# Optimization experiments

Hardware: AMD Instinct MI355X
Metric: run time of the kernel (lower is better)

## Reference

```python
import jax, jax.numpy as jnp
import numpy as np
from jax import lax

TAU = 2.0
VTH = 1.0
T = 4

def heaviside(x):
    return (x >= 0.0).astype(x.dtype)

def lif_step(v, x):
    # decay_input=False, v_reset=0: v <- v*(1-1/tau) + x ; hard reset to 0
    v = v * (1.0 - 1.0 / TAU) + x
    s = heaviside(v - VTH)
    v = v * (1.0 - s)
    return v, s

def setup_inputs() -> dict:
    key = jax.random.key(0)
    k = jax.random.split(key, 5)
    B, H, W3, W4 = 128, 64, 8, 32
    cc, N, O = 8, 512, 16
    flat = cc * H * W3 * W4  # 131072
    x = jax.random.normal(k[0], (B, 2, H, W3, W4), dtype=jnp.float32)
    w_conv = jax.random.normal(k[1], (cc, 2, 3, 3), dtype=jnp.float32) / np.sqrt(2 * 9)
    w1 = jax.random.normal(k[2], (N, flat), dtype=jnp.float32) / np.sqrt(flat)
    w2 = jax.random.normal(k[3], (N, N), dtype=jnp.float32) / np.sqrt(N)
    w_out = jax.random.normal(k[4], (O, N), dtype=jnp.float32) / np.sqrt(N)
    return {"x": x, "w_conv": w_conv, "w1": w1, "w2": w2, "w_out": w_out}

def reference(x, w_conv, w1, w2, w_out):
    B = x.shape[0]
    # input.reshape(B, C, -1, W4)
    xr = x.reshape(B, x.shape[1], -1, x.shape[4])  # (B, 2, 512, 32)
    conv_input = lax.conv_general_dilated(
        xr, w_conv, window_strides=(1, 1), padding="SAME",
        dimension_numbers=("NCHW", "OIHW", "NCHW"))  # (B, cc, 512, 32)

    # lifconv applied T times to the same conv_input with persistent state
    def conv_step(v, _):
        return lif_step(v, conv_input)
    _, conv_spikes = lax.scan(conv_step, jnp.zeros_like(conv_input), None, length=T)  # (T,B,cc,H',W')

    N = w1.shape[0]
    def fc_step(carry, s_conv):
        v1, v2 = carry
        z1 = s_conv.reshape(B, -1) @ w1.T
        v1, s1 = lif_step(v1, z1)
        z2 = s1 @ w2.T
        v2, s2 = lif_step(v2, z2)
        return (v1, v2), (s1, s2)

    v0 = (jnp.zeros((B, N), x.dtype), jnp.zeros((B, N), x.dtype))
    _, (s1_rec, s2_rec) = lax.scan(fc_step, v0, conv_spikes)  # (T,B,N) each

    out = s2_rec.mean(axis=0) @ w_out.T  # (B, O)
    conv_spk_rec = jnp.moveaxis(conv_spikes, 0, 1)   # (B,T,cc,H',W')
    input_spk_rec = jnp.moveaxis(s1_rec, 0, 1)       # (B,T,N)
    hidden_spk_rec = jnp.moveaxis(s2_rec, 0, 1)      # (B,T,N)
    return (out, conv_spk_rec, input_spk_rec, hidden_spk_rec)
```

## Files before the change

### kernel.cpp

```cpp
#include <hip/hip_runtime.h>
#include <stdint.h>


#define OFF_CONV  2048ll
#define OFF_IN    67110912ll
#define OFF_HID   67373056ll

typedef short bf16x8 __attribute__((ext_vector_type(8)));
typedef float f32x4  __attribute__((ext_vector_type(4)));

__device__ __forceinline__ unsigned short f2bf(float f) {
  unsigned u = __float_as_uint(f);
  u += 0x7FFFu + ((u >> 16) & 1u);
  return (unsigned short)(u >> 16);
}

__device__ __forceinline__ void expand2(unsigned x, unsigned& o0, unsigned& o1) {
  o0 = (x & 1u) * 0x3F80u | (x & 0x100u) * 0x3F8000u;
  unsigned y = x >> 16;
  o1 = (y & 1u) * 0x3F80u | (y & 0x100u) * 0x3F8000u;
}

__global__ __launch_bounds__(256) void conv_lif_kernel(
    const float* __restrict__ x, const float* __restrict__ wc,
    float* __restrict__ out, unsigned char* __restrict__ patt)
{
  __shared__ float wcs[144];
  int tid = threadIdx.x;
  if (tid < 144) wcs[tid] = wc[tid];
  __syncthreads();

  int idx = blockIdx.x * 256 + tid;
  int b   = idx >> 15;
  int k4  = idx & 32767;
  int co  = k4 >> 12;
  int rem = k4 & 4095;
  int h   = rem >> 3;
  int w0  = (rem & 7) * 4;

  const float* xb = x + (long long)b * 32768;
  float c[4] = {0.f, 0.f, 0.f, 0.f};
#pragma unroll
  for (int ci = 0; ci < 2; ++ci) {
    const float* xc = xb + ci * 16384;
    const float* wk = wcs + co * 18 + ci * 9;
    float win[3][6];
#pragma unroll
    for (int r = 0; r < 3; ++r) {
      int hh = h - 1 + r;
      if (hh >= 0 && hh < 512) {
        const float* row = xc + hh * 32;
        float4 m = *(const float4*)(row + w0);
        win[r][1] = m.x; win[r][2] = m.y; win[r][3] = m.z; win[r][4] = m.w;
        win[r][0] = (w0 > 0)  ? row[w0 - 1] : 0.f;
        win[r][5] = (w0 < 28) ? row[w0 + 4] : 0.f;
      } else {
#pragma unroll
        for (int j = 0; j < 6; ++j) win[r][j] = 0.f;
      }
    }
#pragma unroll
    for (int r = 0; r < 3; ++r)
#pragma unroll
      for (int dw = 0; dw < 3; ++dw) {
        float wgt = wk[r * 3 + dw];
#pragma unroll
        for (int j = 0; j < 4; ++j) c[j] += win[r][j + dw] * wgt;
      }
  }

  int k = co * 16384 + h * 32 + w0;
  float* ob = out + OFF_CONV + (long long)b * 524288 + k;
  float v[4] = {0.f, 0.f, 0.f, 0.f};
  unsigned p[4] = {0, 0, 0, 0};
#pragma unroll
  for (int t = 0; t < 4; ++t) {
    f32x4 sv;
#pragma unroll
    for (int j = 0; j < 4; ++j) {
      v[j] = v[j] * 0.5f + c[j];
      int si = (v[j] >= 1.0f) ? 1 : 0;
      sv[j] = (float)si;
      if (si) v[j] = 0.f;
      p[j] |= (unsigned)si << t;
    }
    __builtin_nontemporal_store(sv, (f32x4*)(ob + t * 131072));
  }
  unsigned pb = p[0] | (p[1] << 8) | (p[2] << 16) | (p[3] << 24);
  *(unsigned*)(patt + (long long)b * 131072 + k) = pb;
}

__global__ __launch_bounds__(256) void transpose512(
    const float* __restrict__ w2, float* __restrict__ w2t)
{
  __shared__ float tile[32][33];
  int bx = blockIdx.x & 15, by = blockIdx.x >> 4;
  int tx = threadIdx.x & 31, ty = threadIdx.x >> 5;
#pragma unroll
  for (int i = 0; i < 32; i += 8)
    tile[ty + i][tx] = w2[(by * 32 + ty + i) * 512 + bx * 32 + tx];
  __syncthreads();
#pragma unroll
  for (int i = 0; i < 32; i += 8)
    w2t[(bx * 32 + ty + i) * 512 + by * 32 + tx] = tile[tx][ty + i];
}

__global__ __launch_bounds__(512, 4) void gemm_kernel(
    const unsigned char* __restrict__ patt, const float* __restrict__ w1,
    float* __restrict__ partials, int steps)
{
  __shared__ __attribute__((aligned(16))) unsigned short As[4][128][40];
  __shared__ __attribute__((aligned(16))) unsigned short Bh[64][40];
  __shared__ __attribute__((aligned(16))) unsigned short Bl[64][40];

  const int tid   = threadIdx.x;
  const int S     = gridDim.x >> 3;
  const int nt    = blockIdx.x / S;
  const int chunk = blockIdx.x - nt * S;
  const long long k0 = (long long)chunk * steps * 32;

  const int ra  = tid >> 2;
  const int koa = (tid & 3) * 8;
  const unsigned char* pA = patt + (long long)ra * 131072 + k0 + koa;

  const int rb  = tid >> 3;
  const int kob = (tid & 7) * 4;
  const float* pB = w1 + (long long)(nt * 64 + rb) * 131072 + k0 + kob;

  const int lane = tid & 63;
  const int wid  = tid >> 6;
  const int t    = wid >> 1;
  const int mh   = wid & 1;
  const int l15 = lane & 15, quad = lane >> 4;

  f32x4 acc[4][4];
#pragma unroll
  for (int i = 0; i < 4; ++i)
#pragma unroll
    for (int j = 0; j < 4; ++j) acc[i][j] = (f32x4){0.f, 0.f, 0.f, 0.f};

  uint2  pa = *(const uint2*)pA;
  float4 fb = *(const float4*)pB;

  for (int s = 0; s < steps; ++s) {
    uint2 pan = pa; float4 fbn = fb;
    if (s + 1 < steps) {
      pan = *(const uint2*)(pA + (long long)(s + 1) * 32);
      fbn = *(const float4*)(pB + (long long)(s + 1) * 32);
    }

#pragma unroll
    for (int tt = 0; tt < 4; ++tt) {
      unsigned x0 = (pa.x >> tt) & 0x01010101u;
      unsigned x1 = (pa.y >> tt) & 0x01010101u;
      unsigned o0, o1, o2, o3;
      expand2(x0, o0, o1);
      expand2(x1, o2, o3);
      *(uint4*)&As[tt][ra][koa] = make_uint4(o0, o1, o2, o3);
    }

    {
      float fv[4] = {fb.x, fb.y, fb.z, fb.w};
      unsigned hp[2], lp[2];
#pragma unroll
      for (int i = 0; i < 2; ++i) {
        unsigned short h0 = f2bf(fv[2 * i]);
        unsigned short h1 = f2bf(fv[2 * i + 1]);
        float r0 = fv[2 * i]     - __uint_as_float((unsigned)h0 << 16);
        float r1 = fv[2 * i + 1] - __uint_as_float((unsigned)h1 << 16);
        hp[i] = (unsigned)h0 | ((unsigned)h1 << 16);
        lp[i] = (unsigned)f2bf(r0) | ((unsigned)f2bf(r1) << 16);
      }
      *(uint2*)&Bh[rb][kob] = make_uint2(hp[0], hp[1]);
      *(uint2*)&Bl[rb][kob] = make_uint2(lp[0], lp[1]);
    }

    __syncthreads();

    bf16x8 a[4];
#pragma unroll
    for (int f = 0; f < 4; ++f)
      a[f] = *(const bf16x8*)&As[t][mh * 64 + f * 16 + l15][quad * 8];

    __builtin_amdgcn_s_setprio(1);
#pragma unroll
    for (int fn = 0; fn < 4; ++fn) {
      bf16x8 bh = *(const bf16x8*)&Bh[fn * 16 + l15][quad * 8];
      bf16x8 bl = *(const bf16x8*)&Bl[fn * 16 + l15][quad * 8];
#pragma unroll
      for (int fm = 0; fm < 4; ++fm) {
        acc[fm][fn] = __builtin_amdgcn_mfma_f32_16x16x32_bf16(a[fm], bh, acc[fm][fn], 0, 0, 0);
        acc[fm][fn] = __builtin_amdgcn_mfma_f32_16x16x32_bf16(a[fm], bl, acc[fm][fn], 0, 0, 0);
      }
    }
    __builtin_amdgcn_s_setprio(0);

    __syncthreads();

    pa = pan; fb = fbn;
  }

  float* pc = partials + (long long)chunk * 262144;
#pragma unroll
  for (int fm = 0; fm < 4; ++fm)
#pragma unroll
    for (int fn = 0; fn < 4; ++fn) {
      int m = t * 128 + mh * 64 + fm * 16 + quad * 4;
      int n = nt * 64 + fn * 16 + l15;
#pragma unroll
      for (int rg = 0; rg < 4; ++rg)
        pc[(long long)(m + rg) * 512 + n] = acc[fm][fn][rg];
    }
}

__global__ __launch_bounds__(256) void reduce_kernel(
    const float* __restrict__ partials, float* __restrict__ z1, int S)
{
  int idx = (blockIdx.x * 256 + threadIdx.x) * 4;
  float4 a = {0.f, 0.f, 0.f, 0.f};
  for (int c = 0; c < S; ++c) {
    float4 p = *(const float4*)(partials + (long long)c * 262144 + idx);
    a.x += p.x; a.y += p.y; a.z += p.z; a.w += p.w;
  }
  *(float4*)(z1 + idx) = a;
}

__global__ __launch_bounds__(512) void fc_kernel(
    const float* __restrict__ z1, const float* __restrict__ w2t,
    const float* __restrict__ wout, float* __restrict__ out)
{
  int b = blockIdx.x;
  int n = threadIdx.x;
  __shared__ float s1s[512];
  __shared__ float red[512];
  __shared__ unsigned short idxs[512];
  __shared__ int cnts[8];

  const int wid = n >> 6, lane = n & 63;

  float v1 = 0.f, v2 = 0.f, ssum = 0.f;
#pragma unroll
  for (int t = 0; t < 4; ++t) {
    float z = z1[((t * 128 + b) << 9) + n];
    v1 = v1 * 0.5f + z;
    float s1 = (v1 >= 1.0f) ? 1.f : 0.f;
    out[OFF_IN + ((long long)b * 4 + t) * 512 + n] = s1;
    if (s1 != 0.f) v1 = 0.f;

    unsigned long long m = __ballot(s1 != 0.f);
    if (lane == 0) cnts[wid] = __popcll(m);
    __syncthreads();
    int base = 0, total = 0;
#pragma unroll
    for (int w = 0; w < 8; ++w) {
      int c = cnts[w];
      base  += (w < wid) ? c : 0;
      total += c;
    }
    if (s1 != 0.f) {
      int pos = base + (int)__popcll(m & ((1ull << lane) - 1ull));
      idxs[pos] = (unsigned short)n;
    }
    __syncthreads();

    float z2 = 0.f;
    int j = 0;
    for (; j + 8 <= total; j += 8) {
      float a0 = w2t[((int)idxs[j + 0] << 9) + n];
      float a1 = w2t[((int)idxs[j + 1] << 9) + n];
      float a2 = w2t[((int)idxs[j + 2] << 9) + n];
      float a3 = w2t[((int)idxs[j + 3] << 9) + n];
      float a4 = w2t[((int)idxs[j + 4] << 9) + n];
      float a5 = w2t[((int)idxs[j + 5] << 9) + n];
      float a6 = w2t[((int)idxs[j + 6] << 9) + n];
      float a7 = w2t[((int)idxs[j + 7] << 9) + n];
      z2 += a0; z2 += a1; z2 += a2; z2 += a3;
      z2 += a4; z2 += a5; z2 += a6; z2 += a7;
    }
    for (; j < total; ++j)
      z2 += w2t[((int)idxs[j] << 9) + n];

    v2 = v2 * 0.5f + z2;
    float s2 = (v2 >= 1.0f) ? 1.f : 0.f;
    out[OFF_HID + ((long long)b * 4 + t) * 512 + n] = s2;
    if (s2 != 0.f) v2 = 0.f;
    ssum += s2;
    __syncthreads();
  }

  s1s[n] = ssum * 0.25f;
  __syncthreads();

  int o = n & 15, part = n >> 4;
  float p = 0.f;
#pragma unroll
  for (int j = 0; j < 16; ++j)
    p += s1s[part * 16 + j] * wout[o * 512 + part * 16 + j];
  red[n] = p;
  __syncthreads();
  if (n < 16) {
    float a = 0.f;
#pragma unroll
    for (int pp = 0; pp < 32; ++pp) a += red[pp * 16 + n];
    out[b * 16 + n] = a;
  }
}

extern "C" void kernel_launch(void* const* d_in, const int* in_sizes, int n_in,
                              void* d_out, int out_size, void* d_ws, size_t ws_size,
                              hipStream_t stream) {
  const float* x     = (const float*)d_in[0];
  const float* wconv = (const float*)d_in[1];
  const float* w1    = (const float*)d_in[2];
  const float* w2    = (const float*)d_in[3];
  const float* wout  = (const float*)d_in[4];
  float* out = (float*)d_out;
  char* ws = (char*)d_ws;

  unsigned char* patt = (unsigned char*)ws;
  float* w2t      = (float*)(ws + 16777216);
  float* z1       = (float*)(ws + 16777216 + 1048576);
  float* partials = (float*)(ws + 16777216 + 2097152);

  int S = 64;
  while (S > 1 && (size_t)(18874368ull + (size_t)S * 1048576ull) > ws_size) S >>= 1;
  int steps = 4096 / S;

  hipLaunchKernelGGL(conv_lif_kernel, dim3(16384), dim3(256), 0, stream,
                     x, wconv, out, patt);
  hipLaunchKernelGGL(transpose512, dim3(256), dim3(256), 0, stream, w2, w2t);
  hipLaunchKernelGGL(gemm_kernel, dim3(8 * S), dim3(512), 0, stream,
                     patt, w1, partials, steps);
  hipLaunchKernelGGL(reduce_kernel, dim3(256), dim3(256), 0, stream,
                     partials, z1, S);
  hipLaunchKernelGGL(fc_kernel, dim3(128), dim3(512), 0, stream,
                     z1, w2t, wout, out);
}
```

Baseline: 591.3 us.

## Stage packed spike bytes in LDS, expand per wave, and split partial reduction

The GEMM kernel now stores the raw packed 4-timestep spike bytes in shared memory instead of four expanded bf16 copies, and each wave extracts its own timestep bit when it loads A fragments. Blocks drop to 256 threads, with each wave covering 128 rows and holding a larger 8x4 accumulator tile while reusing the B fragments loaded once per step. This is meant to cut LDS footprint and store traffic and to lower the per-block expansion work. The cost is more registers per thread and lower occupancy. The partial-sum reduction is split into two stages so more blocks take part, and it reuses the start of the workspace as scratch for the second stage.

```diff
diff --git a/kernel.cpp b/kernel.cpp
--- a/kernel.cpp
+++ b/kernel.cpp
@@ -105,11 +105,11 @@
     w2t[(bx * 32 + ty + i) * 512 + by * 32 + tx] = tile[tx][ty + i];
 }
 
-__global__ __launch_bounds__(512, 4) void gemm_kernel(
+__global__ __launch_bounds__(256, 2) void gemm_kernel(
     const unsigned char* __restrict__ patt, const float* __restrict__ w1,
     float* __restrict__ partials, int steps)
 {
-  __shared__ __attribute__((aligned(16))) unsigned short As[4][128][40];
+  __shared__ __attribute__((aligned(16))) unsigned char  AsP[128][48];
   __shared__ __attribute__((aligned(16))) unsigned short Bh[64][40];
   __shared__ __attribute__((aligned(16))) unsigned short Bl[64][40];
 
@@ -119,51 +119,43 @@
   const int chunk = blockIdx.x - nt * S;
   const long long k0 = (long long)chunk * steps * 32;
 
-  const int ra  = tid >> 2;
-  const int koa = (tid & 3) * 8;
+  const int ra  = tid >> 1;
+  const int koa = (tid & 1) * 16;
   const unsigned char* pA = patt + (long long)ra * 131072 + k0 + koa;
 
-  const int rb  = tid >> 3;
-  const int kob = (tid & 7) * 4;
+  const int rb  = tid >> 2;
+  const int kob = (tid & 3) * 8;
   const float* pB = w1 + (long long)(nt * 64 + rb) * 131072 + k0 + kob;
 
   const int lane = tid & 63;
-  const int wid  = tid >> 6;
-  const int t    = wid >> 1;
-  const int mh   = wid & 1;
+  const int t    = tid >> 6;
   const int l15 = lane & 15, quad = lane >> 4;
 
-  f32x4 acc[4][4];
-#pragma unroll
-  for (int i = 0; i < 4; ++i)
+  f32x4 acc[8][4];
+#pragma unroll
+  for (int i = 0; i < 8; ++i)
 #pragma unroll
     for (int j = 0; j < 4; ++j) acc[i][j] = (f32x4){0.f, 0.f, 0.f, 0.f};
 
-  uint2  pa = *(const uint2*)pA;
-  float4 fb = *(const float4*)pB;
+  uint4  pa  = *(const uint4*)pA;
+  float4 fb0 = *(const float4*)pB;
+  float4 fb1 = *(const float4*)(pB + 4);
 
   for (int s = 0; s < steps; ++s) {
-    uint2 pan = pa; float4 fbn = fb;
+    uint4 pan = pa; float4 f0n = fb0, f1n = fb1;
     if (s + 1 < steps) {
-      pan = *(const uint2*)(pA + (long long)(s + 1) * 32);
-      fbn = *(const float4*)(pB + (long long)(s + 1) * 32);
-    }
-
-#pragma unroll
-    for (int tt = 0; tt < 4; ++tt) {
-      unsigned x0 = (pa.x >> tt) & 0x01010101u;
-      unsigned x1 = (pa.y >> tt) & 0x01010101u;
-      unsigned o0, o1, o2, o3;
-      expand2(x0, o0, o1);
-      expand2(x1, o2, o3);
-      *(uint4*)&As[tt][ra][koa] = make_uint4(o0, o1, o2, o3);
-    }
+      pan = *(const uint4*)(pA + (long long)(s + 1) * 32);
+      f0n = *(const float4*)(pB + (long long)(s + 1) * 32);
+      f1n = *(const float4*)(pB + (long long)(s + 1) * 32 + 4);
+    }
+
+    *(uint4*)&AsP[ra][koa] = pa;
 
     {
-      float fv[4] = {fb.x, fb.y, fb.z, fb.w};
-      unsigned hp[2], lp[2];
-#pragma unroll
-      for (int i = 0; i < 2; ++i) {
+      float fv[8] = {fb0.x, fb0.y, fb0.z, fb0.w, fb1.x, fb1.y, fb1.z, fb1.w};
+      unsigned hp[4], lp[4];
+#pragma unroll
+      for (int i = 0; i < 4; ++i) {
         unsigned short h0 = f2bf(fv[2 * i]);
         unsigned short h1 = f2bf(fv[2 * i + 1]);
         float r0 = fv[2 * i]     - __uint_as_float((unsigned)h0 << 16);
@@ -171,46 +163,83 @@
         hp[i] = (unsigned)h0 | ((unsigned)h1 << 16);
         lp[i] = (unsigned)f2bf(r0) | ((unsigned)f2bf(r1) << 16);
       }
-      *(uint2*)&Bh[rb][kob] = make_uint2(hp[0], hp[1]);
-      *(uint2*)&Bl[rb][kob] = make_uint2(lp[0], lp[1]);
-    }
-
-    __syncthreads();
-
-    bf16x8 a[4];
-#pragma unroll
-    for (int f = 0; f < 4; ++f)
-      a[f] = *(const bf16x8*)&As[t][mh * 64 + f * 16 + l15][quad * 8];
+      *(uint4*)&Bh[rb][kob] = make_uint4(hp[0], hp[1], hp[2], hp[3]);
+      *(uint4*)&Bl[rb][kob] = make_uint4(lp[0], lp[1], lp[2], lp[3]);
+    }
+
+    __syncthreads();
+
+    bf16x8 bh[4], bl[4];
+#pragma unroll
+    for (int fn = 0; fn < 4; ++fn) {
+      bh[fn] = *(const bf16x8*)&Bh[fn * 16 + l15][quad * 8];
+      bl[fn] = *(const bf16x8*)&Bl[fn * 16 + l15][quad * 8];
+    }
 
     __builtin_amdgcn_s_setprio(1);
 #pragma unroll
+    for (int fm = 0; fm < 8; ++fm) {
+      uint2 ap = *(const uint2*)&AsP[fm * 16 + l15][quad * 8];
+      unsigned x0 = (ap.x >> t) & 0x01010101u;
+      unsigned x1 = (ap.y >> t) & 0x01010101u;
+      unsigned o0, o1, o2, o3;
+      expand2(x0, o0, o1);
+      expand2(x1, o2, o3);
+      union { uint4 u; bf16x8 v; } au;
+      au.u = make_uint4(o0, o1, o2, o3);
+      bf16x8 a = au.v;
+#pragma unroll
+      for (int fn = 0; fn < 4; ++fn) {
+        acc[fm][fn] = __builtin_amdgcn_mfma_f32_16x16x32_bf16(a, bh[fn], acc[fm][fn], 0, 0, 0);
+        acc[fm][fn] = __builtin_amdgcn_mfma_f32_16x16x32_bf16(a, bl[fn], acc[fm][fn], 0, 0, 0);
+      }
+    }
+    __builtin_amdgcn_s_setprio(0);
+
+    __syncthreads();
+
+    pa = pan; fb0 = f0n; fb1 = f1n;
+  }
+
+  float* pc = partials + (long long)chunk * 262144;
+#pragma unroll
+  for (int fm = 0; fm < 8; ++fm)
+#pragma unroll
     for (int fn = 0; fn < 4; ++fn) {
-      bf16x8 bh = *(const bf16x8*)&Bh[fn * 16 + l15][quad * 8];
-      bf16x8 bl = *(const bf16x8*)&Bl[fn * 16 + l15][quad * 8];
-#pragma unroll
-      for (int fm = 0; fm < 4; ++fm) {
-        acc[fm][fn] = __builtin_amdgcn_mfma_f32_16x16x32_bf16(a[fm], bh, acc[fm][fn], 0, 0, 0);
-        acc[fm][fn] = __builtin_amdgcn_mfma_f32_16x16x32_bf16(a[fm], bl, acc[fm][fn], 0, 0, 0);
-      }
-    }
-    __builtin_amdgcn_s_setprio(0);
-
-    __syncthreads();
-
-    pa = pan; fb = fbn;
-  }
-
-  float* pc = partials + (long long)chunk * 262144;
-#pragma unroll
-  for (int fm = 0; fm < 4; ++fm)
-#pragma unroll
-    for (int fn = 0; fn < 4; ++fn) {
-      int m = t * 128 + mh * 64 + fm * 16 + quad * 4;
+      int m = t * 128 + fm * 16 + quad * 4;
       int n = nt * 64 + fn * 16 + l15;
 #pragma unroll
       for (int rg = 0; rg < 4; ++rg)
         pc[(long long)(m + rg) * 512 + n] = acc[fm][fn][rg];
     }
+}
+
+__global__ __launch_bounds__(256) void reduce1_kernel(
+    const float* __restrict__ partials, float* __restrict__ p2)
+{
+  int tg = blockIdx.x * 256 + threadIdx.x;
+  int item = tg & 65535;
+  int g = tg >> 16;
+  const float* src = partials + (long long)g * 8 * 262144 + item * 4;
+  float4 a = {0.f, 0.f, 0.f, 0.f};
+#pragma unroll
+  for (int c = 0; c < 8; ++c) {
+    float4 p = *(const float4*)(src + (long long)c * 262144);
+    a.x += p.x; a.y += p.y; a.z += p.z; a.w += p.w;
+  }
+  *(float4*)(p2 + (long long)g * 262144 + item * 4) = a;
+}
+
+__global__ __launch_bounds__(256) void reduce2_kernel(
+    const float* __restrict__ p2, float* __restrict__ z1, int G)
+{
+  int item = blockIdx.x * 256 + threadIdx.x;
+  float4 a = {0.f, 0.f, 0.f, 0.f};
+  for (int g = 0; g < G; ++g) {
+    float4 p = *(const float4*)(p2 + (long long)g * 262144 + item * 4);
+    a.x += p.x; a.y += p.y; a.z += p.z; a.w += p.w;
+  }
+  *(float4*)(z1 + item * 4) = a;
 }
 
 __global__ __launch_bounds__(256) void reduce_kernel(
@@ -321,6 +350,7 @@
   float* w2t      = (float*)(ws + 16777216);
   float* z1       = (float*)(ws + 16777216 + 1048576);
   float* partials = (float*)(ws + 16777216 + 2097152);
+  float* p2       = (float*)ws;
 
   int S = 64;
   while (S > 1 && (size_t)(18874368ull + (size_t)S * 1048576ull) > ws_size) S >>= 1;
@@ -329,10 +359,18 @@
   hipLaunchKernelGGL(conv_lif_kernel, dim3(16384), dim3(256), 0, stream,
                      x, wconv, out, patt);
   hipLaunchKernelGGL(transpose512, dim3(256), dim3(256), 0, stream, w2, w2t);
-  hipLaunchKernelGGL(gemm_kernel, dim3(8 * S), dim3(512), 0, stream,
+  hipLaunchKernelGGL(gemm_kernel, dim3(8 * S), dim3(256), 0, stream,
                      patt, w1, partials, steps);
-  hipLaunchKernelGGL(reduce_kernel, dim3(256), dim3(256), 0, stream,
-                     partials, z1, S);
+  if (S >= 8) {
+    int G = S / 8;
+    hipLaunchKernelGGL(reduce1_kernel, dim3(G * 256), dim3(256), 0, stream,
+                       partials, p2);
+    hipLaunchKernelGGL(reduce2_kernel, dim3(256), dim3(256), 0, stream,
+                       p2, z1, G);
+  } else {
+    hipLaunchKernelGGL(reduce_kernel, dim3(256), dim3(256), 0, stream,
+                       partials, z1, S);
+  }
   hipLaunchKernelGGL(fc_kernel, dim3(128), dim3(512), 0, stream,
                      z1, w2t, wout, out);
 }
```

Result: no change. 580.6 us (-1.8%).
